# Kernel tuning notes

Measured on AMD Instinct MI355X. Metric: run time of the kernel, lower is better.

Reference implementation:

```python
import jax, jax.numpy as jnp
import numpy as np

N = 50000   # nodes
E = 800000  # edges (before self-loops)
D = 128     # d_model == in_dim
H = 8       # heads
C = D // H  # per-head channels = 16
NEG_SLOPE = 0.2  # PyG GATConv default


def gat_conv(x, row, col, W, a_src, a_dst, bias):
    # x: [N, Din]; row/col: [E'] src/dst with self-loops; W: [Din, H*C]
    h = (x @ W).reshape(N, H, C)                       # [N, H, C]
    alpha_src = (h * a_src).sum(-1)                    # [N, H]
    alpha_dst = (h * a_dst).sum(-1)                    # [N, H]
    e = jax.nn.leaky_relu(alpha_src[row] + alpha_dst[col], NEG_SLOPE)  # [E', H]
    # segment softmax over incoming edges of each dst node (col)
    e_max = jax.ops.segment_max(e, col, num_segments=N)               # [N, H]
    e_exp = jnp.exp(e - e_max[col])                                   # [E', H]
    denom = jax.ops.segment_sum(e_exp, col, num_segments=N)           # [N, H]
    alpha = e_exp / (denom[col] + 1e-16)                              # [E', H]
    msg = h[row] * alpha[:, :, None]                                  # [E', H, C]
    out = jax.ops.segment_sum(msg, col, num_segments=N)               # [N, H, C]
    return out.reshape(N, H * C) + bias


def setup_inputs() -> dict:
    key = jax.random.key(0)
    ks = jax.random.split(key, 14)
    s = 0.05
    return {
        "x": jax.random.normal(ks[0], (N, D), dtype=jnp.float32),
        "edge_index": jax.random.randint(ks[1], (2, E), 0, N, dtype=jnp.int64),
        "pos": jax.random.normal(ks[2], (N, 3), dtype=jnp.float32),
        "W1": jax.random.normal(ks[3], (D, H * C), dtype=jnp.float32) * s,
        "a_src1": jax.random.normal(ks[4], (H, C), dtype=jnp.float32) * s,
        "a_dst1": jax.random.normal(ks[5], (H, C), dtype=jnp.float32) * s,
        "b1": jnp.zeros((H * C,), dtype=jnp.float32),
        "W2": jax.random.normal(ks[6], (D, H * C), dtype=jnp.float32) * s,
        "a_src2": jax.random.normal(ks[7], (H, C), dtype=jnp.float32) * s,
        "a_dst2": jax.random.normal(ks[8], (H, C), dtype=jnp.float32) * s,
        "b2": jnp.zeros((H * C,), dtype=jnp.float32),
        "Wd": jax.random.normal(ks[9], (1, D), dtype=jnp.float32) * s,
        "bd": jnp.zeros((D,), dtype=jnp.float32),
    }


def reference(x, edge_index, pos, W1, a_src1, a_dst1, b1, W2, a_src2, a_dst2, b2, Wd, bd):
    row, col = edge_index[0], edge_index[1]
    # dist embedding (computed in source forward, not used in the returned sum)
    dist = jnp.linalg.norm(pos[row] - pos[col], axis=1, keepdims=True)  # [E, 1]
    dist_emb = jax.nn.relu(dist @ Wd + bd)  # noqa: F841 (unused, as in source)
    # GATConv adds self-loops internally (PyG default add_self_loops=True)
    loop = jnp.arange(N, dtype=row.dtype)
    row_sl = jnp.concatenate([row, loop])
    col_sl = jnp.concatenate([col, loop])
    h1 = jax.nn.relu(gat_conv(x, row_sl, col_sl, W1, a_src1, a_dst1, b1))
    h2 = jax.nn.relu(gat_conv(h1, row_sl, col_sl, W2, a_src2, a_dst2, b2))
    return x + h1 + h2
```

## Files before the change

kernel.cpp:

```cpp
#include <hip/hip_runtime.h>
#include <hip/hip_bf16.h>
#include <math.h>


constexpr int D = 128;
constexpr int CAP = 64;
constexpr int WPACK = 18432;
constexpr int NBMAX = 64;
constexpr int BCAP = 24576;
constexpr int EPB = 4096;

using bf16x8 = __attribute__((ext_vector_type(8))) short;
using f32x4 = __attribute__((ext_vector_type(4))) float;

static __device__ __forceinline__ float lrelu(float v) {
  return v > 0.f ? v : 0.2f * v;
}

static __device__ __forceinline__ ushort bfbits(float f) {
  __hip_bfloat16 b = __float2bfloat16(f);
  return *reinterpret_cast<ushort*>(&b);
}

static __device__ __forceinline__ float bf2f(ushort u) {
  union { unsigned int u; float f; } c;
  c.u = (unsigned int)u << 16;
  return c.f;
}

__global__ void pack_all_kernel(const float* __restrict__ W1, const float* __restrict__ as1,
                                const float* __restrict__ ad1, ushort* __restrict__ wp1,
                                const float* __restrict__ W2, const float* __restrict__ as2,
                                const float* __restrict__ ad2, ushort* __restrict__ wp2,
                                int* __restrict__ bucket_cnt) {
  int t = blockIdx.x * blockDim.x + threadIdx.x;
  if (t < NBMAX) bucket_cnt[t] = 0;
  const float *W, *as_, *ad_;
  ushort* wp;
  int idx;
  if (t < WPACK) {
    W = W1; as_ = as1; ad_ = ad1; wp = wp1; idx = t;
  } else if (t < 2 * WPACK) {
    W = W2; as_ = as2; ad_ = ad2; wp = wp2; idx = t - WPACK;
  } else {
    return;
  }
  if (idx < 16384) {
    int e = idx & 7, c = (idx >> 3) & 15, ct = (idx >> 7) & 7, g = (idx >> 10) & 3,
        ks = idx >> 12;
    int k = ks * 32 + g * 8 + e, n = ct * 16 + c;
    wp[idx] = bfbits(W[k * 128 + n]);
  } else {
    int j = idx - 16384;
    int e = j & 7, c = (j >> 3) & 15, g = (j >> 7) & 3, ks = j >> 9;
    int k = ks * 32 + g * 8 + e;
    int h = c & 7;
    const float* a = (c >> 3) ? ad_ : as_;
    float s = 0.f;
    #pragma unroll
    for (int cc = 0; cc < 16; ++cc) s += W[k * 128 + h * 16 + cc] * a[h * 16 + cc];
    wp[idx] = bfbits(s);
  }
}

__global__ __launch_bounds__(256) void bucket_kernel(
    const int* __restrict__ row, const int* __restrict__ col,
    int* __restrict__ bucket_cnt, unsigned int* __restrict__ bkt, int E, int NB) {
  __shared__ int hist[NBMAX];
  __shared__ int base_s[NBMAX];
  int tid = threadIdx.x;
  if (tid < NBMAX) hist[tid] = 0;
  __syncthreads();
  int e0 = blockIdx.x * EPB;
  unsigned int uv[16];
  int bb[16], rr[16];
  #pragma unroll
  for (int j = 0; j < 16; ++j) {
    int e = e0 + j * 256 + tid;
    bb[j] = -1; uv[j] = 0; rr[j] = 0;
    if (e < E) {
      int c = col[e], r = row[e];
      bb[j] = c >> 10;
      uv[j] = ((unsigned int)(c & 1023) << 16) | (unsigned int)r;
      rr[j] = atomicAdd(&hist[bb[j]], 1);
    }
  }
  __syncthreads();
  if (tid < NB) base_s[tid] = atomicAdd(&bucket_cnt[tid], hist[tid]);
  __syncthreads();
  #pragma unroll
  for (int j = 0; j < 16; ++j) {
    if (bb[j] >= 0) {
      int pos = base_s[bb[j]] + rr[j];
      if (pos < BCAP) bkt[(size_t)bb[j] * BCAP + pos] = uv[j];
    }
  }
}

__global__ __launch_bounds__(256) void csr_gemm_kernel(
    const float* __restrict__ X, const ushort* __restrict__ Wp,
    ushort* __restrict__ Hf, ushort* __restrict__ asrc, float* __restrict__ adst,
    int N, const unsigned int* __restrict__ bkt, const int* __restrict__ bucket_cnt,
    int* __restrict__ cnt, ushort* __restrict__ csr_pad, int NB) {
  __shared__ ushort Wl[WPACK];
  int tid = threadIdx.x;
  if ((int)blockIdx.x < NB) {
    int b = blockIdx.x;
    int* lcnt = (int*)Wl;
    for (int i = tid; i < 1024; i += 256) lcnt[i] = 0;
    __syncthreads();
    int ce = min(bucket_cnt[b], BCAP);
    const unsigned int* bp = bkt + (size_t)b * BCAP;
    for (int i = tid; i < ce; i += 256) {
      unsigned int u = bp[i];
      int dl = u >> 16;
      int p = atomicAdd(&lcnt[dl], 1);
      if (p < CAP) csr_pad[((size_t)((b << 10) + dl)) * CAP + p] = (ushort)(u & 0xffffu);
    }
    __syncthreads();
    int nd = min(1024, N - (b << 10));
    for (int i = tid; i < nd; i += 256) cnt[(b << 10) + i] = lcnt[i];
    return;
  }

  for (int i = tid; i < WPACK / 8; i += 256)
    *(uint4*)&Wl[i * 8] = *(const uint4*)&Wp[i * 8];
  __syncthreads();

  int lane = tid & 63, w = tid >> 6;
  int g = lane >> 4, c = lane & 15;
  int rt0 = ((int)blockIdx.x - NB) * 128 + w * 32;

  f32x4 acc[2][9];
  #pragma unroll
  for (int rt = 0; rt < 2; ++rt)
    #pragma unroll
    for (int ct = 0; ct < 9; ++ct) acc[rt][ct] = (f32x4)0.f;

  #pragma unroll
  for (int ks = 0; ks < 4; ++ks) {
    bf16x8 a[2];
    #pragma unroll
    for (int rt = 0; rt < 2; ++rt) {
      int r = rt0 + rt * 16 + c;
      if (r < N) {
        const float* xp = &X[(size_t)r * D + ks * 32 + g * 8];
        float4 x0 = *(const float4*)xp;
        float4 x1 = *(const float4*)(xp + 4);
        bf16x8 t;
        t[0] = (short)bfbits(x0.x); t[1] = (short)bfbits(x0.y);
        t[2] = (short)bfbits(x0.z); t[3] = (short)bfbits(x0.w);
        t[4] = (short)bfbits(x1.x); t[5] = (short)bfbits(x1.y);
        t[6] = (short)bfbits(x1.z); t[7] = (short)bfbits(x1.w);
        a[rt] = t;
      } else {
        a[rt] = (bf16x8)(short)0;
      }
    }
    #pragma unroll
    for (int ct = 0; ct < 9; ++ct) {
      const ushort* bp = (ct < 8)
          ? &Wl[(size_t)(((ks * 4 + g) * 8 + ct) * 16 + c) * 8]
          : &Wl[16384 + (size_t)((ks * 4 + g) * 16 + c) * 8];
      bf16x8 b = *(const bf16x8*)bp;
      acc[0][ct] = __builtin_amdgcn_mfma_f32_16x16x32_bf16(a[0], b, acc[0][ct], 0, 0, 0);
      acc[1][ct] = __builtin_amdgcn_mfma_f32_16x16x32_bf16(a[1], b, acc[1][ct], 0, 0, 0);
    }
  }

  #pragma unroll
  for (int rt = 0; rt < 2; ++rt) {
    #pragma unroll
    for (int j = 0; j < 4; ++j) {
      int r = rt0 + rt * 16 + g * 4 + j;
      if (r >= N) continue;
      #pragma unroll
      for (int ct = 0; ct < 8; ++ct)
        Hf[(size_t)r * D + ct * 16 + c] = bfbits(acc[rt][ct][j]);
      float lv = acc[rt][8][j];
      if (c < 8) asrc[r * 8 + c] = bfbits(lv);
      else adst[r * 8 + (c - 8)] = lv;
    }
  }
}

static __device__ __forceinline__ void gather_node(
    const ushort* __restrict__ Hf, const ushort* __restrict__ asrc, float adst_h,
    const int* __restrict__ cnt, const ushort* __restrict__ csr_pad,
    int dst, int h, int d0, float& accx, float& accy, float& wsum) {
  float ws = __expf(lrelu(bf2f(asrc[dst * 8 + h]) + adst_h));
  ushort2 fs = *(const ushort2*)&Hf[(size_t)dst * D + d0];
  accx = ws * bf2f(fs.x); accy = ws * bf2f(fs.y); wsum = ws;
  int cn = min(cnt[dst], CAP);
  const ushort* cp = csr_pad + (size_t)dst * CAP;
  int i = 0;
  for (; i + 4 <= cn; i += 4) {
    ushort4 s4 = *(const ushort4*)(cp + i);
    float l0 = bf2f(asrc[(int)s4.x * 8 + h]);
    float l1 = bf2f(asrc[(int)s4.y * 8 + h]);
    float l2 = bf2f(asrc[(int)s4.z * 8 + h]);
    float l3 = bf2f(asrc[(int)s4.w * 8 + h]);
    ushort2 f0 = *(const ushort2*)&Hf[(size_t)s4.x * D + d0];
    ushort2 f1 = *(const ushort2*)&Hf[(size_t)s4.y * D + d0];
    ushort2 f2 = *(const ushort2*)&Hf[(size_t)s4.z * D + d0];
    ushort2 f3 = *(const ushort2*)&Hf[(size_t)s4.w * D + d0];
    float w0 = __expf(lrelu(l0 + adst_h));
    float w1 = __expf(lrelu(l1 + adst_h));
    float w2 = __expf(lrelu(l2 + adst_h));
    float w3 = __expf(lrelu(l3 + adst_h));
    accx += w0 * bf2f(f0.x) + w1 * bf2f(f1.x) + w2 * bf2f(f2.x) + w3 * bf2f(f3.x);
    accy += w0 * bf2f(f0.y) + w1 * bf2f(f1.y) + w2 * bf2f(f2.y) + w3 * bf2f(f3.y);
    wsum += w0 + w1 + w2 + w3;
  }
  for (; i < cn; ++i) {
    int src = cp[i];
    float we = __expf(lrelu(bf2f(asrc[src * 8 + h]) + adst_h));
    ushort2 fv = *(const ushort2*)&Hf[(size_t)src * D + d0];
    accx += we * bf2f(fv.x);
    accy += we * bf2f(fv.y);
    wsum += we;
  }
}

__global__ __launch_bounds__(256) void agg_gemm_kernel(
    const ushort* __restrict__ Hf1, const ushort* __restrict__ asrc1,
    const float* __restrict__ adst1, const int* __restrict__ cnt,
    const ushort* __restrict__ csr_pad, const float* __restrict__ bias1,
    const ushort* __restrict__ wp2, ushort* __restrict__ h1out,
    ushort* __restrict__ Hf2, ushort* __restrict__ asrc2, float* __restrict__ adst2,
    int N) {
  __shared__ ushort Ht[32][144];
  int tid = threadIdx.x, lane = tid & 63, w = tid >> 6;
  int h = lane >> 3, d0 = lane * 2;
  int dst0 = blockIdx.x * 32;

  for (int i = 0; i < 8; ++i) {
    int trow = w * 8 + i;
    int dst = dst0 + trow;
    float r0 = 0.f, r1 = 0.f;
    if (dst < N) {
      float adh = adst1[dst * 8 + h];
      float ax, ay, wsm;
      gather_node(Hf1, asrc1, adh, cnt, csr_pad, dst, h, d0, ax, ay, wsm);
      float inv = 1.f / (wsm + 1e-16f);
      float2 bv = *(const float2*)&bias1[d0];
      r0 = fmaxf(ax * inv + bv.x, 0.f);
      r1 = fmaxf(ay * inv + bv.y, 0.f);
    }
    ushort2 u;
    u.x = bfbits(r0); u.y = bfbits(r1);
    *(ushort2*)&Ht[trow][d0] = u;
    if (dst < N) *(ushort2*)&h1out[(size_t)dst * D + d0] = u;
  }
  __syncthreads();

  int g = lane >> 4, c = lane & 15;
  bf16x8 afr[2][4];
  #pragma unroll
  for (int rt = 0; rt < 2; ++rt)
    #pragma unroll
    for (int ks = 0; ks < 4; ++ks)
      afr[rt][ks] = *(const bf16x8*)&Ht[rt * 16 + c][ks * 32 + g * 8];

  f32x4 acc[2][3];
  #pragma unroll
  for (int rt = 0; rt < 2; ++rt)
    #pragma unroll
    for (int ci = 0; ci < 3; ++ci) acc[rt][ci] = (f32x4)0.f;

  #pragma unroll
  for (int ci = 0; ci < 3; ++ci) {
    bool act = (ci < 2) || (w == 0);
    if (!act) continue;
    int ct = (ci == 0) ? w : (ci == 1) ? (4 + w) : 8;
    #pragma unroll
    for (int ks = 0; ks < 4; ++ks) {
      const ushort* bp = (ct < 8)
          ? &wp2[(size_t)(((ks * 4 + g) * 8 + ct) * 16 + c) * 8]
          : &wp2[16384 + (size_t)((ks * 4 + g) * 16 + c) * 8];
      bf16x8 b = *(const bf16x8*)bp;
      acc[0][ci] = __builtin_amdgcn_mfma_f32_16x16x32_bf16(afr[0][ks], b, acc[0][ci], 0, 0, 0);
      acc[1][ci] = __builtin_amdgcn_mfma_f32_16x16x32_bf16(afr[1][ks], b, acc[1][ci], 0, 0, 0);
    }
  }

  #pragma unroll
  for (int ci = 0; ci < 3; ++ci) {
    bool act = (ci < 2) || (w == 0);
    if (!act) continue;
    int ct = (ci == 0) ? w : (ci == 1) ? (4 + w) : 8;
    #pragma unroll
    for (int rt = 0; rt < 2; ++rt) {
      #pragma unroll
      for (int j = 0; j < 4; ++j) {
        int r = rt * 16 + g * 4 + j;
        int dst = dst0 + r;
        if (dst >= N) continue;
        float lv = acc[rt][ci][j];
        if (ct < 8) {
          Hf2[(size_t)dst * D + ct * 16 + c] = bfbits(lv);
        } else {
          if (c < 8) asrc2[dst * 8 + c] = bfbits(lv);
          else adst2[dst * 8 + (c - 8)] = lv;
        }
      }
    }
  }
}

__global__ __launch_bounds__(256) void aggregate2_kernel(
    const ushort* __restrict__ Hf, const ushort* __restrict__ asrc,
    const float* __restrict__ adst, const int* __restrict__ cnt,
    const ushort* __restrict__ csr_pad, const float* __restrict__ bias,
    const float* __restrict__ xin, const ushort* __restrict__ h1in,
    float* __restrict__ outp, int N) {
  int wid = (blockIdx.x * blockDim.x + threadIdx.x) >> 6;
  if (wid >= N) return;
  int lane = threadIdx.x & 63;
  int h = lane >> 3, d0 = lane * 2;
  int dst = wid;
  float adh = adst[dst * 8 + h];
  float ax, ay, wsm;
  gather_node(Hf, asrc, adh, cnt, csr_pad, dst, h, d0, ax, ay, wsm);
  float inv = 1.f / (wsm + 1e-16f);
  float2 bv = *(const float2*)&bias[d0];
  float r0 = fmaxf(ax * inv + bv.x, 0.f);
  float r1 = fmaxf(ay * inv + bv.y, 0.f);
  float2 xv = *(const float2*)&xin[(size_t)dst * D + d0];
  ushort2 hv = *(const ushort2*)&h1in[(size_t)dst * D + d0];
  *(float2*)&outp[(size_t)dst * D + d0] =
      make_float2(xv.x + bf2f(hv.x) + r0, xv.y + bf2f(hv.y) + r1);
}

extern "C" void kernel_launch(void* const* d_in, const int* in_sizes, int n_in,
                              void* d_out, int out_size, void* d_ws, size_t ws_size,
                              hipStream_t stream) {
  const float* x = (const float*)d_in[0];
  const int* ei = (const int*)d_in[1];
  const float* W1 = (const float*)d_in[3];
  const float* as1 = (const float*)d_in[4];
  const float* ad1 = (const float*)d_in[5];
  const float* b1 = (const float*)d_in[6];
  const float* W2 = (const float*)d_in[7];
  const float* as2 = (const float*)d_in[8];
  const float* ad2 = (const float*)d_in[9];
  const float* b2 = (const float*)d_in[10];
  float* out = (float*)d_out;

  const int N = in_sizes[0] / D;
  const int E = in_sizes[1] / 2;
  const int* row = ei;
  const int* col = ei + E;
  const int NB = (N + 1023) >> 10;

  char* base = (char*)d_ws;
  size_t o = 0;
  auto alloc = [&](size_t bytes) {
    void* p = base + o;
    o = (o + bytes + 255) & ~(size_t)255;
    return p;
  };
  int* bucket_cnt = (int*)alloc((size_t)NBMAX * 4);
  unsigned int* bkt = (unsigned int*)alloc((size_t)NBMAX * BCAP * 4);
  int* cnt = (int*)alloc((size_t)N * 4);
  ushort* csr_pad = (ushort*)alloc((size_t)N * CAP * 2);
  ushort* hf1 = (ushort*)alloc((size_t)N * D * 2);
  ushort* hf2 = (ushort*)alloc((size_t)N * D * 2);
  ushort* h1 = (ushort*)alloc((size_t)N * D * 2);
  ushort* asrc1 = (ushort*)alloc((size_t)N * 8 * 2);
  ushort* asrc2 = (ushort*)alloc((size_t)N * 8 * 2);
  float* adst1 = (float*)alloc((size_t)N * 8 * 4);
  float* adst2 = (float*)alloc((size_t)N * 8 * 4);
  ushort* wp1 = (ushort*)alloc((size_t)WPACK * 2);
  ushort* wp2 = (ushort*)alloc((size_t)WPACK * 2);

  int gemm_blocks = (N + 127) / 128;

  pack_all_kernel<<<(2 * WPACK + 255) / 256, 256, 0, stream>>>(
      W1, as1, ad1, wp1, W2, as2, ad2, wp2, bucket_cnt);
  bucket_kernel<<<(E + EPB - 1) / EPB, 256, 0, stream>>>(row, col, bucket_cnt, bkt, E, NB);
  csr_gemm_kernel<<<NB + gemm_blocks, 256, 0, stream>>>(
      x, wp1, hf1, asrc1, adst1, N, bkt, bucket_cnt, cnt, csr_pad, NB);
  agg_gemm_kernel<<<(N + 31) / 32, 256, 0, stream>>>(
      hf1, asrc1, adst1, cnt, csr_pad, b1, wp2, h1, hf2, asrc2, adst2, N);
  aggregate2_kernel<<<(N + 3) / 4, 256, 0, stream>>>(
      hf2, asrc2, adst2, cnt, csr_pad, b2, x, h1, out, N);
}
```

Measured before the change: 260.3 us.

## Split fused layer-1 aggregate+GEMM into separate aggregate and GEMM kernels

Replaces the fused aggregation-plus-layer-2-GEMM kernel with a one-wavefront-per-node aggregate kernel (templated per layer) followed by a standalone MFMA GEMM kernel that stages packed weights in LDS. Feature and attention buffers are reused across layers. The gather loop also gains an 8-wide unrolled path that issues all index-dependent loads before the exp/accumulate work, to raise memory-level parallelism. The split adds an extra launch and a round trip of h1 through global memory. In exchange it removes the serialised per-wave 8-node loop and the block barrier in the fused kernel.

```diff
diff --git a/kernel.cpp b/kernel.cpp
--- a/kernel.cpp
+++ b/kernel.cpp
@@ -184,6 +184,62 @@
   }
 }
 
+__global__ __launch_bounds__(256) void gemm2_kernel(
+    const ushort* __restrict__ Xv, const ushort* __restrict__ Wp,
+    ushort* __restrict__ Hf, ushort* __restrict__ asrc, float* __restrict__ adst,
+    int N) {
+  __shared__ ushort Wl[WPACK];
+  int tid = threadIdx.x;
+  for (int i = tid; i < WPACK / 8; i += 256)
+    *(uint4*)&Wl[i * 8] = *(const uint4*)&Wp[i * 8];
+  __syncthreads();
+
+  int lane = tid & 63, w = tid >> 6;
+  int g = lane >> 4, c = lane & 15;
+  int rt0 = blockIdx.x * 128 + w * 32;
+
+  f32x4 acc[2][9];
+  #pragma unroll
+  for (int rt = 0; rt < 2; ++rt)
+    #pragma unroll
+    for (int ct = 0; ct < 9; ++ct) acc[rt][ct] = (f32x4)0.f;
+
+  #pragma unroll
+  for (int ks = 0; ks < 4; ++ks) {
+    bf16x8 a[2];
+    #pragma unroll
+    for (int rt = 0; rt < 2; ++rt) {
+      int r = rt0 + rt * 16 + c;
+      a[rt] = (r < N) ? *(const bf16x8*)&Xv[(size_t)r * D + ks * 32 + g * 8]
+                      : (bf16x8)(short)0;
+    }
+    #pragma unroll
+    for (int ct = 0; ct < 9; ++ct) {
+      const ushort* bp = (ct < 8)
+          ? &Wl[(size_t)(((ks * 4 + g) * 8 + ct) * 16 + c) * 8]
+          : &Wl[16384 + (size_t)((ks * 4 + g) * 16 + c) * 8];
+      bf16x8 b = *(const bf16x8*)bp;
+      acc[0][ct] = __builtin_amdgcn_mfma_f32_16x16x32_bf16(a[0], b, acc[0][ct], 0, 0, 0);
+      acc[1][ct] = __builtin_amdgcn_mfma_f32_16x16x32_bf16(a[1], b, acc[1][ct], 0, 0, 0);
+    }
+  }
+
+  #pragma unroll
+  for (int rt = 0; rt < 2; ++rt) {
+    #pragma unroll
+    for (int j = 0; j < 4; ++j) {
+      int r = rt0 + rt * 16 + g * 4 + j;
+      if (r >= N) continue;
+      #pragma unroll
+      for (int ct = 0; ct < 8; ++ct)
+        Hf[(size_t)r * D + ct * 16 + c] = bfbits(acc[rt][ct][j]);
+      float lv = acc[rt][8][j];
+      if (c < 8) asrc[r * 8 + c] = bfbits(lv);
+      else adst[r * 8 + (c - 8)] = lv;
+    }
+  }
+}
+
 static __device__ __forceinline__ void gather_node(
     const ushort* __restrict__ Hf, const ushort* __restrict__ asrc, float adst_h,
     const int* __restrict__ cnt, const ushort* __restrict__ csr_pad,
@@ -194,23 +250,40 @@
   int cn = min(cnt[dst], CAP);
   const ushort* cp = csr_pad + (size_t)dst * CAP;
   int i = 0;
+  for (; i + 8 <= cn; i += 8) {
+    ushort4 sa = *(const ushort4*)(cp + i);
+    ushort4 sb = *(const ushort4*)(cp + i + 4);
+    int s[8] = {sa.x, sa.y, sa.z, sa.w, sb.x, sb.y, sb.z, sb.w};
+    float l[8];
+    ushort2 f[8];
+    #pragma unroll
+    for (int j = 0; j < 8; ++j) l[j] = bf2f(asrc[s[j] * 8 + h]);
+    #pragma unroll
+    for (int j = 0; j < 8; ++j) f[j] = *(const ushort2*)&Hf[(size_t)s[j] * D + d0];
+    #pragma unroll
+    for (int j = 0; j < 8; ++j) {
+      float we = __expf(lrelu(l[j] + adst_h));
+      accx += we * bf2f(f[j].x);
+      accy += we * bf2f(f[j].y);
+      wsum += we;
+    }
+  }
   for (; i + 4 <= cn; i += 4) {
     ushort4 s4 = *(const ushort4*)(cp + i);
-    float l0 = bf2f(asrc[(int)s4.x * 8 + h]);
-    float l1 = bf2f(asrc[(int)s4.y * 8 + h]);
-    float l2 = bf2f(asrc[(int)s4.z * 8 + h]);
-    float l3 = bf2f(asrc[(int)s4.w * 8 + h]);
-    ushort2 f0 = *(const ushort2*)&Hf[(size_t)s4.x * D + d0];
-    ushort2 f1 = *(const ushort2*)&Hf[(size_t)s4.y * D + d0];
-    ushort2 f2 = *(const ushort2*)&Hf[(size_t)s4.z * D + d0];
-    ushort2 f3 = *(const ushort2*)&Hf[(size_t)s4.w * D + d0];
-    float w0 = __expf(lrelu(l0 + adst_h));
-    float w1 = __expf(lrelu(l1 + adst_h));
-    float w2 = __expf(lrelu(l2 + adst_h));
-    float w3 = __expf(lrelu(l3 + adst_h));
-    accx += w0 * bf2f(f0.x) + w1 * bf2f(f1.x) + w2 * bf2f(f2.x) + w3 * bf2f(f3.x);
-    accy += w0 * bf2f(f0.y) + w1 * bf2f(f1.y) + w2 * bf2f(f2.y) + w3 * bf2f(f3.y);
-    wsum += w0 + w1 + w2 + w3;
+    int s[4] = {s4.x, s4.y, s4.z, s4.w};
+    float l[4];
+    ushort2 f[4];
+    #pragma unroll
+    for (int j = 0; j < 4; ++j) l[j] = bf2f(asrc[s[j] * 8 + h]);
+    #pragma unroll
+    for (int j = 0; j < 4; ++j) f[j] = *(const ushort2*)&Hf[(size_t)s[j] * D + d0];
+    #pragma unroll
+    for (int j = 0; j < 4; ++j) {
+      float we = __expf(lrelu(l[j] + adst_h));
+      accx += we * bf2f(f[j].x);
+      accy += we * bf2f(f[j].y);
+      wsum += we;
+    }
   }
   for (; i < cn; ++i) {
     int src = cp[i];
@@ -222,98 +295,13 @@
   }
 }
 
-__global__ __launch_bounds__(256) void agg_gemm_kernel(
-    const ushort* __restrict__ Hf1, const ushort* __restrict__ asrc1,
-    const float* __restrict__ adst1, const int* __restrict__ cnt,
-    const ushort* __restrict__ csr_pad, const float* __restrict__ bias1,
-    const ushort* __restrict__ wp2, ushort* __restrict__ h1out,
-    ushort* __restrict__ Hf2, ushort* __restrict__ asrc2, float* __restrict__ adst2,
-    int N) {
-  __shared__ ushort Ht[32][144];
-  int tid = threadIdx.x, lane = tid & 63, w = tid >> 6;
-  int h = lane >> 3, d0 = lane * 2;
-  int dst0 = blockIdx.x * 32;
-
-  for (int i = 0; i < 8; ++i) {
-    int trow = w * 8 + i;
-    int dst = dst0 + trow;
-    float r0 = 0.f, r1 = 0.f;
-    if (dst < N) {
-      float adh = adst1[dst * 8 + h];
-      float ax, ay, wsm;
-      gather_node(Hf1, asrc1, adh, cnt, csr_pad, dst, h, d0, ax, ay, wsm);
-      float inv = 1.f / (wsm + 1e-16f);
-      float2 bv = *(const float2*)&bias1[d0];
-      r0 = fmaxf(ax * inv + bv.x, 0.f);
-      r1 = fmaxf(ay * inv + bv.y, 0.f);
-    }
-    ushort2 u;
-    u.x = bfbits(r0); u.y = bfbits(r1);
-    *(ushort2*)&Ht[trow][d0] = u;
-    if (dst < N) *(ushort2*)&h1out[(size_t)dst * D + d0] = u;
-  }
-  __syncthreads();
-
-  int g = lane >> 4, c = lane & 15;
-  bf16x8 afr[2][4];
-  #pragma unroll
-  for (int rt = 0; rt < 2; ++rt)
-    #pragma unroll
-    for (int ks = 0; ks < 4; ++ks)
-      afr[rt][ks] = *(const bf16x8*)&Ht[rt * 16 + c][ks * 32 + g * 8];
-
-  f32x4 acc[2][3];
-  #pragma unroll
-  for (int rt = 0; rt < 2; ++rt)
-    #pragma unroll
-    for (int ci = 0; ci < 3; ++ci) acc[rt][ci] = (f32x4)0.f;
-
-  #pragma unroll
-  for (int ci = 0; ci < 3; ++ci) {
-    bool act = (ci < 2) || (w == 0);
-    if (!act) continue;
-    int ct = (ci == 0) ? w : (ci == 1) ? (4 + w) : 8;
-    #pragma unroll
-    for (int ks = 0; ks < 4; ++ks) {
-      const ushort* bp = (ct < 8)
-          ? &wp2[(size_t)(((ks * 4 + g) * 8 + ct) * 16 + c) * 8]
-          : &wp2[16384 + (size_t)((ks * 4 + g) * 16 + c) * 8];
-      bf16x8 b = *(const bf16x8*)bp;
-      acc[0][ci] = __builtin_amdgcn_mfma_f32_16x16x32_bf16(afr[0][ks], b, acc[0][ci], 0, 0, 0);
-      acc[1][ci] = __builtin_amdgcn_mfma_f32_16x16x32_bf16(afr[1][ks], b, acc[1][ci], 0, 0, 0);
-    }
-  }
-
-  #pragma unroll
-  for (int ci = 0; ci < 3; ++ci) {
-    bool act = (ci < 2) || (w == 0);
-    if (!act) continue;
-    int ct = (ci == 0) ? w : (ci == 1) ? (4 + w) : 8;
-    #pragma unroll
-    for (int rt = 0; rt < 2; ++rt) {
-      #pragma unroll
-      for (int j = 0; j < 4; ++j) {
-        int r = rt * 16 + g * 4 + j;
-        int dst = dst0 + r;
-        if (dst >= N) continue;
-        float lv = acc[rt][ci][j];
-        if (ct < 8) {
-          Hf2[(size_t)dst * D + ct * 16 + c] = bfbits(lv);
-        } else {
-          if (c < 8) asrc2[dst * 8 + c] = bfbits(lv);
-          else adst2[dst * 8 + (c - 8)] = lv;
-        }
-      }
-    }
-  }
-}
-
-__global__ __launch_bounds__(256) void aggregate2_kernel(
+template <int LAYER>
+__global__ __launch_bounds__(256) void aggregate_kernel(
     const ushort* __restrict__ Hf, const ushort* __restrict__ asrc,
     const float* __restrict__ adst, const int* __restrict__ cnt,
     const ushort* __restrict__ csr_pad, const float* __restrict__ bias,
     const float* __restrict__ xin, const ushort* __restrict__ h1in,
-    float* __restrict__ outp, int N) {
+    void* __restrict__ outp, int N) {
   int wid = (blockIdx.x * blockDim.x + threadIdx.x) >> 6;
   if (wid >= N) return;
   int lane = threadIdx.x & 63;
@@ -326,10 +314,16 @@
   float2 bv = *(const float2*)&bias[d0];
   float r0 = fmaxf(ax * inv + bv.x, 0.f);
   float r1 = fmaxf(ay * inv + bv.y, 0.f);
-  float2 xv = *(const float2*)&xin[(size_t)dst * D + d0];
-  ushort2 hv = *(const ushort2*)&h1in[(size_t)dst * D + d0];
-  *(float2*)&outp[(size_t)dst * D + d0] =
-      make_float2(xv.x + bf2f(hv.x) + r0, xv.y + bf2f(hv.y) + r1);
+  if (LAYER == 1) {
+    ushort2 u;
+    u.x = bfbits(r0); u.y = bfbits(r1);
+    *(ushort2*)&((ushort*)outp)[(size_t)dst * D + d0] = u;
+  } else {
+    float2 xv = *(const float2*)&xin[(size_t)dst * D + d0];
+    ushort2 hv = *(const ushort2*)&h1in[(size_t)dst * D + d0];
+    *(float2*)&((float*)outp)[(size_t)dst * D + d0] =
+        make_float2(xv.x + bf2f(hv.x) + r0, xv.y + bf2f(hv.y) + r1);
+  }
 }
 
 extern "C" void kernel_launch(void* const* d_in, const int* in_sizes, int n_in,
@@ -364,25 +358,24 @@
   unsigned int* bkt = (unsigned int*)alloc((size_t)NBMAX * BCAP * 4);
   int* cnt = (int*)alloc((size_t)N * 4);
   ushort* csr_pad = (ushort*)alloc((size_t)N * CAP * 2);
-  ushort* hf1 = (ushort*)alloc((size_t)N * D * 2);
-  ushort* hf2 = (ushort*)alloc((size_t)N * D * 2);
+  ushort* hf = (ushort*)alloc((size_t)N * D * 2);
   ushort* h1 = (ushort*)alloc((size_t)N * D * 2);
-  ushort* asrc1 = (ushort*)alloc((size_t)N * 8 * 2);
-  ushort* asrc2 = (ushort*)alloc((size_t)N * 8 * 2);
-  float* adst1 = (float*)alloc((size_t)N * 8 * 4);
-  float* adst2 = (float*)alloc((size_t)N * 8 * 4);
+  ushort* asrcb = (ushort*)alloc((size_t)N * 8 * 2);
+  float* adstb = (float*)alloc((size_t)N * 8 * 4);
   ushort* wp1 = (ushort*)alloc((size_t)WPACK * 2);
   ushort* wp2 = (ushort*)alloc((size_t)WPACK * 2);
 
   int gemm_blocks = (N + 127) / 128;
+  int agg_blocks = (N + 3) / 4;
 
   pack_all_kernel<<<(2 * WPACK + 255) / 256, 256, 0, stream>>>(
       W1, as1, ad1, wp1, W2, as2, ad2, wp2, bucket_cnt);
   bucket_kernel<<<(E + EPB - 1) / EPB, 256, 0, stream>>>(row, col, bucket_cnt, bkt, E, NB);
   csr_gemm_kernel<<<NB + gemm_blocks, 256, 0, stream>>>(
-      x, wp1, hf1, asrc1, adst1, N, bkt, bucket_cnt, cnt, csr_pad, NB);
-  agg_gemm_kernel<<<(N + 31) / 32, 256, 0, stream>>>(
-      hf1, asrc1, adst1, cnt, csr_pad, b1, wp2, h1, hf2, asrc2, adst2, N);
-  aggregate2_kernel<<<(N + 3) / 4, 256, 0, stream>>>(
-      hf2, asrc2, adst2, cnt, csr_pad, b2, x, h1, out, N);
-}
+      x, wp1, hf, asrcb, adstb, N, bkt, bucket_cnt, cnt, csr_pad, NB);
+  aggregate_kernel<1><<<agg_blocks, 256, 0, stream>>>(
+      hf, asrcb, adstb, cnt, csr_pad, b1, nullptr, nullptr, h1, N);
+  gemm2_kernel<<<gemm_blocks, 256, 0, stream>>>(h1, wp2, hf, asrcb, adstb, N);
+  aggregate_kernel<2><<<agg_blocks, 256, 0, stream>>>(
+      hf, asrcb, adstb, cnt, csr_pad, b2, x, h1, out, N);
+}
```

Measured after the change: 230.4 us. 11.5% less time.
